# Optimization experiments

Hardware: AMD Instinct MI355X
Metric: run time of the kernel (lower is better)

The kernel has to match this reference:

```python
import jax, jax.numpy as jnp
import numpy as np

N_PAPER, N_AUTHOR, N_SUBJECT = 100000, 50000, 5000
N_INP, N_HID, N_OUT = 256, 128, 16
E_PA, E_AP, E_PS, E_SP = 600000, 600000, 200000, 200000


def _seg_mean(msg, dst, n_dst):
    # segment-sum over destination nodes, normalized by in-degree (mean agg)
    s = jax.ops.segment_sum(msg, dst, num_segments=n_dst)
    deg = jax.ops.segment_sum(jnp.ones((dst.shape[0],), msg.dtype), dst, num_segments=n_dst)
    return s / jnp.maximum(deg, 1.0)[:, None]


def _rel_conv(x_src, w, src, dst, n_dst):
    # transform-then-gather (fewer FLOPs than gather-then-transform)
    m = (x_src @ w)[src]  # [E, n_hid]
    return _seg_mean(m, dst, n_dst)


def setup_inputs() -> dict:
    key = jax.random.key(0)
    ks = jax.random.split(key, 32)
    s = 0.05
    inp = {
        'x_paper': jax.random.normal(ks[0], (N_PAPER, N_INP), jnp.float32),
        'x_author': jax.random.normal(ks[1], (N_AUTHOR, N_INP), jnp.float32),
        'x_subject': jax.random.normal(ks[2], (N_SUBJECT, N_INP), jnp.float32),
        'pa_src': jax.random.randint(ks[3], (E_PA,), 0, N_PAPER),
        'pa_dst': jax.random.randint(ks[4], (E_PA,), 0, N_AUTHOR),
        'ap_src': jax.random.randint(ks[5], (E_AP,), 0, N_AUTHOR),
        'ap_dst': jax.random.randint(ks[6], (E_AP,), 0, N_PAPER),
        'ps_src': jax.random.randint(ks[7], (E_PS,), 0, N_PAPER),
        'ps_dst': jax.random.randint(ks[8], (E_PS,), 0, N_SUBJECT),
        'sp_src': jax.random.randint(ks[9], (E_SP,), 0, N_SUBJECT),
        'sp_dst': jax.random.randint(ks[10], (E_SP,), 0, N_PAPER),
        # HeteroAdaptMLP params (per node type, n_layer=1, gelu)
        'enc_w_paper': jax.random.normal(ks[11], (N_INP, N_HID), jnp.float32) * s,
        'enc_b_paper': jnp.zeros((N_HID,), jnp.float32),
        'enc_w_author': jax.random.normal(ks[12], (N_INP, N_HID), jnp.float32) * s,
        'enc_b_author': jnp.zeros((N_HID,), jnp.float32),
        'enc_w_subject': jax.random.normal(ks[13], (N_INP, N_HID), jnp.float32) * s,
        'enc_b_subject': jnp.zeros((N_HID,), jnp.float32),
        # per-relation GraphConv weights, 2 layers x 4 relations
        'w0_pa': jax.random.normal(ks[14], (N_HID, N_HID), jnp.float32) * s,
        'w0_ap': jax.random.normal(ks[15], (N_HID, N_HID), jnp.float32) * s,
        'w0_ps': jax.random.normal(ks[16], (N_HID, N_HID), jnp.float32) * s,
        'w0_sp': jax.random.normal(ks[17], (N_HID, N_HID), jnp.float32) * s,
        'w1_pa': jax.random.normal(ks[18], (N_HID, N_HID), jnp.float32) * s,
        'w1_ap': jax.random.normal(ks[19], (N_HID, N_HID), jnp.float32) * s,
        'w1_ps': jax.random.normal(ks[20], (N_HID, N_HID), jnp.float32) * s,
        'w1_sp': jax.random.normal(ks[21], (N_HID, N_HID), jnp.float32) * s,
        # output head
        'out_w': jax.random.normal(ks[22], (N_HID, N_OUT), jnp.float32) * s,
        'out_b': jnp.zeros((N_OUT,), jnp.float32),
    }
    return inp


def reference(x_paper, x_author, x_subject,
              pa_src, pa_dst, ap_src, ap_dst, ps_src, ps_dst, sp_src, sp_dst,
              enc_w_paper, enc_b_paper, enc_w_author, enc_b_author,
              enc_w_subject, enc_b_subject,
              w0_pa, w0_ap, w0_ps, w0_sp, w1_pa, w1_ap, w1_ps, w1_sp,
              out_w, out_b):
    # task_specific_encoder: per-node-type 1-layer MLP with gelu
    h_p = jax.nn.gelu(x_paper @ enc_w_paper + enc_b_paper)
    h_a = jax.nn.gelu(x_author @ enc_w_author + enc_b_author)
    h_s = jax.nn.gelu(x_subject @ enc_w_subject + enc_b_subject)

    for (w_pa, w_ap, w_ps, w_sp) in ((w0_pa, w0_ap, w0_ps, w0_sp),
                                     (w1_pa, w1_ap, w1_ps, w1_sp)):
        # per-relation gather -> GraphConv(mean) -> scatter; 'sum' across relations
        new_a = _rel_conv(h_p, w_pa, pa_src, pa_dst, N_AUTHOR)
        new_s = _rel_conv(h_p, w_ps, ps_src, ps_dst, N_SUBJECT)
        new_p = (_rel_conv(h_a, w_ap, ap_src, ap_dst, N_PAPER)
                 + _rel_conv(h_s, w_sp, sp_src, sp_dst, N_PAPER))
        # activation=None, self_loop=False, dropout is identity at inference
        h_p, h_a, h_s = new_p, new_a, new_s

    # out_key = 'paper'
    return h_p @ out_w + out_b
```

## Files before the change

### kernel.cpp

```cpp
#include <hip/hip_runtime.h>
#include <math.h>

constexpr int NP = 100000, NA = 50000, NS = 5000;
constexpr int EPA = 600000, EAP = 600000, EPS = 200000, ESP = 200000;
constexpr int ETOT = EPA + EPS + EAP + ESP;
constexpr int NT   = NA + NS + NP + NP;
constexpr int OFF_PS = EPA, OFF_AP = EPA + EPS, OFF_SP = EPA + EPS + EAP;
constexpr int ROW_PS = NA, ROW_AP = NA + NS, ROW_SP = NA + NS + NP;

constexpr int CAP_PA = 48;
constexpr int CAP_PS = 96;
constexpr int CAP_AP = 32;
constexpr int CAP_SP = 24;

constexpr int NB_FOLD  = 2;
constexpr int NB_PACK  = (256*128)/256;
constexpr int NB_ENC   = (NP + 63)/64;
constexpr int NB_HIST  = (ETOT/2 + 255)/256;
constexpr int NB_HE    = 3*NB_ENC;
constexpr int NB_FILLB = ((ETOT-OFF_AP)+1023)/1024;
constexpr int NB_G16   = ((NA+NS)*16 + 255)/256;

typedef short s16x8 __attribute__((ext_vector_type(8)));
typedef float f32x4 __attribute__((ext_vector_type(4)));
typedef unsigned short u16;

__device__ __forceinline__ float gelu_f(float x) {
  float x3 = x*x*x;
  return 0.5f*x*(1.0f + tanhf(0.7978845608028654f*(x + 0.044715f*x3)));
}
__device__ __forceinline__ u16 f2bf(float f) {
  unsigned u = __float_as_uint(f);
  u += 0x7fffu + ((u >> 16) & 1u);
  return (u16)(u >> 16);
}

__global__ __launch_bounds__(256) void fold_pack(
    const float* __restrict__ w0_pa, const float* __restrict__ w1_ap,
    const float* __restrict__ w0_ps, const float* __restrict__ w1_sp,
    const float* __restrict__ out_w, u16* __restrict__ WFb,
    const float* __restrict__ ewp, u16* __restrict__ wpk)
{
  __shared__ float Wst[64*132];
  __shared__ float OW[128*16];
  __shared__ float U[128*16];
  const int b = blockIdx.x, tid = threadIdx.x;

  if (b >= NB_FOLD) {
    int o = (b - NB_FOLD)*256 + tid;
    int bb = o & 7;
    int l  = (o >> 3) & 63;
    int cf = (o >> 9) & 7;
    int ks = o >> 12;
    wpk[o] = f2bf(ewp[(ks*32 + (l>>4)*8 + bb)*128 + cf*16 + (l & 15)]);
    return;
  }

  const float* w0 = (b == 0) ? w0_pa : w0_ps;
  const float* w1 = (b == 0) ? w1_ap : w1_sp;
  for (int i = tid; i < 512; i += 256) ((float4*)OW)[i] = ((const float4*)out_w)[i];
  for (int half = 0; half < 2; ++half) {
    __syncthreads();
    for (int i = tid; i < 64*32; i += 256) {
      int row = i >> 5, q = i & 31;
      float4 v = ((const float4*)(w1 + (size_t)(half*64 + row)*128))[q];
      *(float4*)&Wst[row*132 + q*4] = v;
    }
    __syncthreads();
    #pragma unroll
    for (int i = 0; i < 4; ++i) {
      int idx = tid + 256*i;
      int r = idx >> 4, c = idx & 15;
      float acc = 0.f;
      #pragma unroll 8
      for (int k = 0; k < 128; ++k) acc = fmaf(Wst[r*132+k], OW[k*16+c], acc);
      U[(half*64 + r)*16 + c] = acc;
    }
  }
  for (int half = 0; half < 2; ++half) {
    __syncthreads();
    for (int i = tid; i < 64*32; i += 256) {
      int row = i >> 5, q = i & 31;
      float4 v = ((const float4*)(w0 + (size_t)(half*64 + row)*128))[q];
      *(float4*)&Wst[row*132 + q*4] = v;
    }
    __syncthreads();
    #pragma unroll
    for (int i = 0; i < 4; ++i) {
      int idx = tid + 256*i;
      int r = idx >> 4, c = idx & 15;
      float acc = 0.f;
      #pragma unroll 8
      for (int k = 0; k < 128; ++k) acc = fmaf(Wst[r*132+k], U[k*16+c], acc);
      int k = half*64 + r;
      int ks = k >> 5;
      int lane = (((k >> 3) & 3) << 4) | c;
      WFb[(((size_t)ks*2 + b)*64 + lane)*8 + (k & 7)] = f2bf(acc);
    }
  }
}

__global__ __launch_bounds__(256) void hist_enc(
    const int* __restrict__ pa_d, const int* __restrict__ ps_d,
    const int* __restrict__ ap_d, const int* __restrict__ sp_d,
    int* __restrict__ h, u16* __restrict__ rank16,
    const float* __restrict__ A, const u16* __restrict__ Wp,
    const float* __restrict__ bias, const u16* __restrict__ WFb,
    float* __restrict__ YZ)
{
  __shared__ u16 xs[64*264];
  const int b = blockIdx.x;
  const int tid = threadIdx.x;

  if (b % 3 != 2) {
    const int hb = (b/3)*2 + (b%3);
    const int e = (hb*256 + tid)*2;
    if (e >= ETOT) return;
    const int* dsts; int off;
    if (e < OFF_PS)      { dsts = pa_d;          off = 0; }
    else if (e < OFF_AP) { dsts = ps_d - OFF_PS; off = ROW_PS; }
    else if (e < OFF_SP) { dsts = ap_d - OFF_AP; off = ROW_AP; }
    else                 { dsts = sp_d - OFF_SP; off = ROW_SP; }
    int2 d2 = *(const int2*)(dsts + e);
    unsigned p0 = (unsigned)atomicAdd(&h[(size_t)(off + d2.x) << 2], 1);
    unsigned p1 = (unsigned)atomicAdd(&h[(size_t)(off + d2.y) << 2], 1);
    *(unsigned*)(rank16 + e) = (p0 & 0xffffu) | (p1 << 16);
    return;
  }

  const int eb = b / 3;
  const int rowbase = eb*64;
  const int lane = tid & 63, wv = tid >> 6;
  const int m = lane & 15, kq = lane >> 4;

  s16x8 breg[8][2];
  #pragma unroll
  for (int ks = 0; ks < 8; ++ks) {
    breg[ks][0] = ((const s16x8*)Wp)[(ks*8 + 2*wv + 0)*64 + lane];
    breg[ks][1] = ((const s16x8*)Wp)[(ks*8 + 2*wv + 1)*64 + lane];
  }

  #pragma unroll
  for (int i = 0; i < 16; ++i) {
    int idx = i*256 + tid;
    int row = idx >> 6, c4 = idx & 63;
    int grow = rowbase + row;
    float4 v = make_float4(0.f,0.f,0.f,0.f);
    if (grow < NP) v = *(const float4*)(A + (size_t)grow*256 + c4*4);
    ushort4 bv;
    bv.x = f2bf(v.x); bv.y = f2bf(v.y); bv.z = f2bf(v.z); bv.w = f2bf(v.w);
    *(ushort4*)&xs[row*264 + c4*4] = bv;
  }
  __syncthreads();

  f32x4 acc[4][2];
  #pragma unroll
  for (int t = 0; t < 4; ++t) { acc[t][0] = (f32x4){0.f,0.f,0.f,0.f}; acc[t][1] = (f32x4){0.f,0.f,0.f,0.f}; }
  #pragma unroll
  for (int t = 0; t < 4; ++t)
    #pragma unroll
    for (int ks = 0; ks < 8; ++ks) {
      s16x8 a0 = *(const s16x8*)&xs[(t*16 + m)*264 + ks*32 + kq*8];
      acc[t][0] = __builtin_amdgcn_mfma_f32_16x16x32_bf16(a0, breg[ks][0], acc[t][0], 0, 0, 0);
      acc[t][1] = __builtin_amdgcn_mfma_f32_16x16x32_bf16(a0, breg[ks][1], acc[t][1], 0, 0, 0);
    }
  __syncthreads();

  #pragma unroll
  for (int t = 0; t < 4; ++t)
    #pragma unroll
    for (int c = 0; c < 2; ++c) {
      const int col = (2*wv + c)*16 + m;
      const float bcol = bias[col];
      #pragma unroll
      for (int r = 0; r < 4; ++r)
        xs[(t*16 + kq*4 + r)*264 + col] = f2bf(gelu_f(acc[t][c][r] + bcol));
    }
  __syncthreads();

  const s16x8* WFv = (const s16x8*)WFb;
  f32x4 y0 = (f32x4){0.f,0.f,0.f,0.f};
  f32x4 y1 = (f32x4){0.f,0.f,0.f,0.f};
  #pragma unroll
  for (int ks = 0; ks < 4; ++ks) {
    s16x8 af = *(const s16x8*)&xs[(wv*16 + m)*264 + ks*32 + kq*8];
    y0 = __builtin_amdgcn_mfma_f32_16x16x32_bf16(af, WFv[(ks*2+0)*64 + lane], y0, 0, 0, 0);
    y1 = __builtin_amdgcn_mfma_f32_16x16x32_bf16(af, WFv[(ks*2+1)*64 + lane], y1, 0, 0, 0);
  }
  #pragma unroll
  for (int r = 0; r < 4; ++r) {
    const int row = rowbase + wv*16 + kq*4 + r;
    if (row < NP) {
      YZ[(size_t)row*32 + m]      = y0[r];
      YZ[(size_t)row*32 + 16 + m] = y1[r];
    }
  }
}

__global__ void fill_paps(
    const int* __restrict__ pa_s, const int* __restrict__ pa_d,
    const int* __restrict__ ps_s, const int* __restrict__ ps_d,
    const u16* __restrict__ rank16,
    int* __restrict__ ci_pa, int* __restrict__ ci_ps)
{
  int e = (blockIdx.x*256 + threadIdx.x)*4;
  if (e >= OFF_AP) return;
  const int *srcs, *dsts; int cap; int* ci;
  if (e < OFF_PS) { srcs = pa_s;          dsts = pa_d;          cap = CAP_PA; ci = ci_pa; }
  else            { srcs = ps_s - OFF_PS; dsts = ps_d - OFF_PS; cap = CAP_PS; ci = ci_ps; }
  int4 s4 = *(const int4*)(srcs + e);
  int4 d4 = *(const int4*)(dsts + e);
  uint2 rr = *(const uint2*)(rank16 + e);
  int r0 = (int)(rr.x & 0xffffu), r1 = (int)(rr.x >> 16);
  int r2 = (int)(rr.y & 0xffffu), r3 = (int)(rr.y >> 16);
  if (r0 < cap) ci[d4.x*cap + r0] = s4.x;
  if (r1 < cap) ci[d4.y*cap + r1] = s4.y;
  if (r2 < cap) ci[d4.z*cap + r2] = s4.z;
  if (r3 < cap) ci[d4.w*cap + r3] = s4.w;
}

__global__ __launch_bounds__(256) void g16_fill(
    const float* __restrict__ yz, const int* __restrict__ h,
    const int* __restrict__ ci_pa, const int* __restrict__ ci_ps,
    float* __restrict__ m16,
    const int* __restrict__ ap_s, const int* __restrict__ ap_d,
    const int* __restrict__ sp_s, const int* __restrict__ sp_d,
    const u16* __restrict__ rank16,
    int* __restrict__ ci_ap, int* __restrict__ ci_sp)
{
  const int b = blockIdx.x;
  if (b < NB_FILLB) {
    int e = OFF_AP + (b*256 + (int)threadIdx.x)*4;
    if (e >= ETOT) return;
    const int *srcs, *dsts; int cap; int* ci;
    if (e < OFF_SP) { srcs = ap_s - OFF_AP; dsts = ap_d - OFF_AP; cap = CAP_AP; ci = ci_ap; }
    else            { srcs = sp_s - OFF_SP; dsts = sp_d - OFF_SP; cap = CAP_SP; ci = ci_sp; }
    int4 s4 = *(const int4*)(srcs + e);
    int4 d4 = *(const int4*)(dsts + e);
    uint2 rr = *(const uint2*)(rank16 + e);
    int r0 = (int)(rr.x & 0xffffu), r1 = (int)(rr.x >> 16);
    int r2 = (int)(rr.y & 0xffffu), r3 = (int)(rr.y >> 16);
    if (r0 < cap) ci[d4.x*cap + r0] = s4.x;
    if (r1 < cap) ci[d4.y*cap + r1] = s4.y;
    if (r2 < cap) ci[d4.z*cap + r2] = s4.z;
    if (r3 < cap) ci[d4.w*cap + r3] = s4.w;
    return;
  }
  int t = (b - NB_FILLB)*256 + threadIdx.x;
  int row = t >> 4, lane = t & 15;
  if (row >= NA + NS) return;
  const int* ci; int deg, cap, off;
  if (row < NA) { deg = h[(size_t)row << 2];            ci = ci_pa + (size_t)row*CAP_PA; cap = CAP_PA; off = lane; }
  else          { int s = row - NA;
                  deg = h[(size_t)(ROW_PS + s) << 2];   ci = ci_ps + (size_t)s*CAP_PS;   cap = CAP_PS; off = 16 + lane; }
  int n = deg < cap ? deg : cap;
  float a = 0.f, bb = 0.f;
  int k = 0;
  for (; k + 1 < n; k += 2) {
    a  += yz[(size_t)ci[k]  *32 + off];
    bb += yz[(size_t)ci[k+1]*32 + off];
  }
  if (k < n) a += yz[(size_t)ci[k]*32 + off];
  m16[(size_t)row*16 + lane] = (a + bb) / (float)(deg > 0 ? deg : 1);
}

__global__ __launch_bounds__(256) void gather2_16(const float* __restrict__ m16,
    const int* __restrict__ h,
    const int* __restrict__ ci_ap, const int* __restrict__ ci_sp,
    const float* __restrict__ ob, float* __restrict__ O)
{
  int t = blockIdx.x*256 + threadIdx.x;
  int row = t >> 4, lane = t & 15;
  if (row >= NP) return;

  const float* fa = m16;
  const float* fs = m16 + (size_t)NA*16;

  float s1 = 0.f, s1b = 0.f;
  {
    int deg = h[(size_t)(ROW_AP + row) << 2];
    int n = deg < CAP_AP ? deg : CAP_AP;
    const int* c1 = ci_ap + (size_t)row*CAP_AP;
    int k = 0;
    for (; k + 1 < n; k += 2) {
      s1  += fa[(size_t)c1[k]  *16 + lane];
      s1b += fa[(size_t)c1[k+1]*16 + lane];
    }
    if (k < n) s1 += fa[(size_t)c1[k]*16 + lane];
    s1 = (s1 + s1b) / (float)(deg > 0 ? deg : 1);
  }
  float s2 = 0.f, s2b = 0.f;
  {
    int deg = h[(size_t)(ROW_SP + row) << 2];
    int n = deg < CAP_SP ? deg : CAP_SP;
    const int* c2 = ci_sp + (size_t)row*CAP_SP;
    int k = 0;
    for (; k + 1 < n; k += 2) {
      s2  += fs[(size_t)c2[k]  *16 + lane];
      s2b += fs[(size_t)c2[k+1]*16 + lane];
    }
    if (k < n) s2 += fs[(size_t)c2[k]*16 + lane];
    s2 = (s2 + s2b) / (float)(deg > 0 ? deg : 1);
  }
  O[(size_t)row*16 + lane] = s1 + s2 + ob[lane];
}

extern "C" void kernel_launch(void* const* d_in, const int* in_sizes, int n_in,
                              void* d_out, int out_size, void* d_ws, size_t ws_size,
                              hipStream_t stream)
{
  const float* x_p = (const float*)d_in[0];
  const int* pa_src=(const int*)d_in[3]; const int* pa_dst=(const int*)d_in[4];
  const int* ap_src=(const int*)d_in[5]; const int* ap_dst=(const int*)d_in[6];
  const int* ps_src=(const int*)d_in[7]; const int* ps_dst=(const int*)d_in[8];
  const int* sp_src=(const int*)d_in[9]; const int* sp_dst=(const int*)d_in[10];
  const float* ewp=(const float*)d_in[11]; const float* ebp=(const float*)d_in[12];
  const float* w0_pa=(const float*)d_in[17];
  const float* w0_ps=(const float*)d_in[19];
  const float* w1_ap=(const float*)d_in[22];
  const float* w1_sp=(const float*)d_in[24];
  const float* out_w=(const float*)d_in[25]; const float* out_b=(const float*)d_in[26];
  float* out = (float*)d_out;

  char* wp = (char*)d_ws;
  auto alloc = [&](size_t bytes) { char* p = wp; wp += (bytes + 255) & ~(size_t)255; return p; };
  float* yz     = (float*)alloc((size_t)NP*32*4);
  float* m16    = (float*)alloc((size_t)(NA+NS)*16*4);
  u16*   wpk    = (u16*)alloc((size_t)256*128*2);
  u16*   WFb    = (u16*)alloc((size_t)8*64*8*2);
  int*   h      = (int*)alloc((size_t)NT*16);
  u16*   rank16 = (u16*)alloc((size_t)ETOT*2);
  int*   ci_pa  = (int*)alloc((size_t)NA*CAP_PA*4);
  int*   ci_ps  = (int*)alloc((size_t)NS*CAP_PS*4);
  int*   ci_ap  = (int*)alloc((size_t)NP*CAP_AP*4);
  int*   ci_sp  = (int*)alloc((size_t)NP*CAP_SP*4);

  hipMemsetAsync(h, 0, (size_t)NT*16, stream);
  fold_pack<<<NB_FOLD+NB_PACK,256,0,stream>>>(
      w0_pa, w1_ap, w0_ps, w1_sp, out_w, WFb, ewp, wpk);

  hist_enc<<<NB_HE,256,0,stream>>>(
      pa_dst, ps_dst, ap_dst, sp_dst, h, rank16,
      x_p, wpk, ebp, WFb, yz);

  fill_paps<<<(OFF_AP+1023)/1024,256,0,stream>>>(
      pa_src, pa_dst, ps_src, ps_dst, rank16, ci_pa, ci_ps);

  g16_fill<<<NB_FILLB+NB_G16,256,0,stream>>>(
      yz, h, ci_pa, ci_ps, m16,
      ap_src, ap_dst, sp_src, sp_dst, rank16, ci_ap, ci_sp);

  gather2_16<<<(((size_t)NP*16)+255)/256,256,0,stream>>>(m16, h, ci_ap, ci_sp, out_b, out);
}
```

Measured before the change: 184.9 us.

## Rebalance histogram work: move ap/sp degree counting into the fill kernel

The first fused kernel now interleaves only the pa/ps histogram atomics with the encoder MFMA blocks. The ap/sp histogram atomics move into the next kernel, where they are interleaved with the pa/ps CSR fill blocks. The aim is to balance work across the two launches so the atomic-heavy histogram overlaps with fill scatter instead of all stacking on the encoder kernel. Block counts are hard-coded (3*782), which must match the edge counts for correctness.

```diff
diff --git a/kernel.cpp b/kernel.cpp
--- a/kernel.cpp
+++ b/kernel.cpp
@@ -16,8 +16,8 @@
 constexpr int NB_FOLD  = 2;
 constexpr int NB_PACK  = (256*128)/256;
 constexpr int NB_ENC   = (NP + 63)/64;
-constexpr int NB_HIST  = (ETOT/2 + 255)/256;
-constexpr int NB_HE    = 3*NB_ENC;
+constexpr int NB_K1    = 2*NB_ENC;
+constexpr int NB_K2    = 3*782;
 constexpr int NB_FILLB = ((ETOT-OFF_AP)+1023)/1024;
 constexpr int NB_G16   = ((NA+NS)*16 + 255)/256;
 
@@ -102,7 +102,6 @@
 
 __global__ __launch_bounds__(256) void hist_enc(
     const int* __restrict__ pa_d, const int* __restrict__ ps_d,
-    const int* __restrict__ ap_d, const int* __restrict__ sp_d,
     int* __restrict__ h, u16* __restrict__ rank16,
     const float* __restrict__ A, const u16* __restrict__ Wp,
     const float* __restrict__ bias, const u16* __restrict__ WFb,
@@ -112,15 +111,12 @@
   const int b = blockIdx.x;
   const int tid = threadIdx.x;
 
-  if (b % 3 != 2) {
-    const int hb = (b/3)*2 + (b%3);
-    const int e = (hb*256 + tid)*2;
-    if (e >= ETOT) return;
+  if (!(b & 1)) {
+    const int e = ((b >> 1)*256 + tid)*2;
+    if (e >= OFF_AP) return;
     const int* dsts; int off;
-    if (e < OFF_PS)      { dsts = pa_d;          off = 0; }
-    else if (e < OFF_AP) { dsts = ps_d - OFF_PS; off = ROW_PS; }
-    else if (e < OFF_SP) { dsts = ap_d - OFF_AP; off = ROW_AP; }
-    else                 { dsts = sp_d - OFF_SP; off = ROW_SP; }
+    if (e < OFF_PS) { dsts = pa_d;          off = 0; }
+    else            { dsts = ps_d - OFF_PS; off = ROW_PS; }
     int2 d2 = *(const int2*)(dsts + e);
     unsigned p0 = (unsigned)atomicAdd(&h[(size_t)(off + d2.x) << 2], 1);
     unsigned p1 = (unsigned)atomicAdd(&h[(size_t)(off + d2.y) << 2], 1);
@@ -128,7 +124,7 @@
     return;
   }
 
-  const int eb = b / 3;
+  const int eb = b >> 1;
   const int rowbase = eb*64;
   const int lane = tid & 63, wv = tid >> 6;
   const int m = lane & 15, kq = lane >> 4;
@@ -197,26 +193,44 @@
   }
 }
 
-__global__ void fill_paps(
+__global__ void hist_fill(
+    const int* __restrict__ ap_d, const int* __restrict__ sp_d,
+    int* __restrict__ h, u16* __restrict__ rank16,
     const int* __restrict__ pa_s, const int* __restrict__ pa_d,
     const int* __restrict__ ps_s, const int* __restrict__ ps_d,
-    const u16* __restrict__ rank16,
     int* __restrict__ ci_pa, int* __restrict__ ci_ps)
 {
-  int e = (blockIdx.x*256 + threadIdx.x)*4;
-  if (e >= OFF_AP) return;
-  const int *srcs, *dsts; int cap; int* ci;
-  if (e < OFF_PS) { srcs = pa_s;          dsts = pa_d;          cap = CAP_PA; ci = ci_pa; }
-  else            { srcs = ps_s - OFF_PS; dsts = ps_d - OFF_PS; cap = CAP_PS; ci = ci_ps; }
-  int4 s4 = *(const int4*)(srcs + e);
-  int4 d4 = *(const int4*)(dsts + e);
-  uint2 rr = *(const uint2*)(rank16 + e);
-  int r0 = (int)(rr.x & 0xffffu), r1 = (int)(rr.x >> 16);
-  int r2 = (int)(rr.y & 0xffffu), r3 = (int)(rr.y >> 16);
-  if (r0 < cap) ci[d4.x*cap + r0] = s4.x;
-  if (r1 < cap) ci[d4.y*cap + r1] = s4.y;
-  if (r2 < cap) ci[d4.z*cap + r2] = s4.z;
-  if (r3 < cap) ci[d4.w*cap + r3] = s4.w;
+  const int b = blockIdx.x;
+  const int tid = threadIdx.x;
+
+  if (b % 3 == 2) {
+    int e = ((b/3)*256 + tid)*4;
+    if (e >= OFF_AP) return;
+    const int *srcs, *dsts; int cap; int* ci;
+    if (e < OFF_PS) { srcs = pa_s;          dsts = pa_d;          cap = CAP_PA; ci = ci_pa; }
+    else            { srcs = ps_s - OFF_PS; dsts = ps_d - OFF_PS; cap = CAP_PS; ci = ci_ps; }
+    int4 s4 = *(const int4*)(srcs + e);
+    int4 d4 = *(const int4*)(dsts + e);
+    uint2 rr = *(const uint2*)(rank16 + e);
+    int r0 = (int)(rr.x & 0xffffu), r1 = (int)(rr.x >> 16);
+    int r2 = (int)(rr.y & 0xffffu), r3 = (int)(rr.y >> 16);
+    if (r0 < cap) ci[d4.x*cap + r0] = s4.x;
+    if (r1 < cap) ci[d4.y*cap + r1] = s4.y;
+    if (r2 < cap) ci[d4.z*cap + r2] = s4.z;
+    if (r3 < cap) ci[d4.w*cap + r3] = s4.w;
+    return;
+  }
+
+  const int hb = (b/3)*2 + (b%3);
+  const int e = OFF_AP + (hb*256 + tid)*2;
+  if (e >= ETOT) return;
+  const int* dsts; int off;
+  if (e < OFF_SP) { dsts = ap_d - OFF_AP; off = ROW_AP; }
+  else            { dsts = sp_d - OFF_SP; off = ROW_SP; }
+  int2 d2 = *(const int2*)(dsts + e);
+  unsigned p0 = (unsigned)atomicAdd(&h[(size_t)(off + d2.x) << 2], 1);
+  unsigned p1 = (unsigned)atomicAdd(&h[(size_t)(off + d2.y) << 2], 1);
+  *(unsigned*)(rank16 + e) = (p0 & 0xffffu) | (p1 << 16);
 }
 
 __global__ __launch_bounds__(256) void g16_fill(
@@ -339,12 +353,13 @@
   fold_pack<<<NB_FOLD+NB_PACK,256,0,stream>>>(
       w0_pa, w1_ap, w0_ps, w1_sp, out_w, WFb, ewp, wpk);
 
-  hist_enc<<<NB_HE,256,0,stream>>>(
-      pa_dst, ps_dst, ap_dst, sp_dst, h, rank16,
+  hist_enc<<<NB_K1,256,0,stream>>>(
+      pa_dst, ps_dst, h, rank16,
       x_p, wpk, ebp, WFb, yz);
 
-  fill_paps<<<(OFF_AP+1023)/1024,256,0,stream>>>(
-      pa_src, pa_dst, ps_src, ps_dst, rank16, ci_pa, ci_ps);
+  hist_fill<<<NB_K2,256,0,stream>>>(
+      ap_dst, sp_dst, h, rank16,
+      pa_src, pa_dst, ps_src, ps_dst, ci_pa, ci_ps);
 
   g16_fill<<<NB_FILLB+NB_G16,256,0,stream>>>(
       yz, h, ci_pa, ci_ps, m16,
```

Result: slower. 205.2 us (+11.0%).
